# Performance work log

Hardware: AMD Instinct MI355X
Metric: run time of the kernel (lower is better)

Reference implementation:

```python
import jax, jax.numpy as jnp
import numpy as np

B, N, M, LDIM, RDIM, AGG = 4, 512, 512, 512, 512, 256


def setup_inputs() -> dict:
    key = jax.random.key(0)
    ks = jax.random.split(key, 7)
    data = jax.random.normal(ks[0], (B, N, LDIM), dtype=jnp.float32)
    crit = jax.random.normal(ks[1], (B, M, RDIM), dtype=jnp.float32)
    Wl = jax.random.normal(ks[2], (LDIM, AGG), dtype=jnp.float32) / np.sqrt(LDIM)
    bl = jax.random.normal(ks[3], (AGG,), dtype=jnp.float32) * 0.01
    Wr = jax.random.normal(ks[4], (RDIM, AGG), dtype=jnp.float32) / np.sqrt(RDIM)
    br = jax.random.normal(ks[5], (AGG,), dtype=jnp.float32) * 0.01
    agg = jax.random.uniform(ks[6], (AGG,), dtype=jnp.float32, minval=-0.01, maxval=0.01)
    return {"data": data, "crit": crit, "Wl": Wl, "bl": bl, "Wr": Wr, "br": br, "agg": agg}


def reference(data, crit, Wl, bl, Wr, br, agg):
    # linear projections
    datalin = jnp.einsum('bnl,la->bna', data, Wl) + bl   # [B,N,A]
    critlin = jnp.einsum('bmr,ra->bma', crit, Wr) + br   # [B,M,A]
    # broadcast add -> tanh -> reduce with agg vector: [B,N,M]
    linsum = jnp.tanh(datalin[:, :, None, :] + critlin[:, None, :, :])  # [B,N,M,A]
    dists = jnp.einsum('bnma,a->bnm', linsum, agg)
    return dists
```

## Files before the change

kernel.cpp:

```cpp
#include <hip/hip_runtime.h>


#define A_DIM 256
#define K_DIM 512
#define NROWS 2048

typedef unsigned short ushort;
typedef __attribute__((ext_vector_type(4))) unsigned short us4;

__device__ inline ushort f2bf(float x) {
    union { float f; unsigned u; } v; v.f = x;
    unsigned r = v.u + 0x7FFFu + ((v.u >> 16) & 1u);
    return (ushort)(r >> 16);
}
__device__ inline float bf2f(ushort h) {
    union { unsigned u; float f; } v; v.u = ((unsigned)h) << 16; return v.f;
}

__global__ __launch_bounds__(256) void proj_exp_kernel(
    const float* __restrict__ data, const float* __restrict__ crit,
    const float* __restrict__ Wl, const float* __restrict__ bl,
    const float* __restrict__ Wr, const float* __restrict__ br,
    ushort* __restrict__ ws16)
{
    __shared__ __align__(16) float Xs[16][68];
    __shared__ __align__(16) float Wsm[16][64];

    const int t   = threadIdx.x;
    const int bid = blockIdx.x;
    const int ct  = bid & 3;
    const int rt  = (bid >> 2) & 31;
    const int kh  = (bid >> 7) & 1;
    const int src = bid >> 8;

    const int r0 = rt * 64, c0 = ct * 64, kb = kh * 256;
    const float* X    = src ? crit : data;
    const float* W    = src ? Wr   : Wl;
    const float* bias = src ? br   : bl;
    ushort* ET = ws16 + (size_t)(src * 2 + kh) * ((size_t)A_DIM * NROWS);

    const int tx = t & 15;
    const int ty = t >> 4;
    const int sr = t >> 2;
    const int sk = (t & 3) * 4;
    const int wk = t >> 4;
    const int wc = (t & 15) * 4;

    float acc[4][4];
#pragma unroll
    for (int i = 0; i < 4; i++)
#pragma unroll
        for (int j = 0; j < 4; j++) acc[i][j] = 0.f;

    for (int k0 = 0; k0 < 256; k0 += 16) {
        float4 xv = *(const float4*)(X + (size_t)(r0 + sr) * K_DIM + kb + k0 + sk);
        float4 wv = *(const float4*)(W + (size_t)(kb + k0 + wk) * A_DIM + c0 + wc);
        __syncthreads();
        Xs[sk + 0][sr] = xv.x; Xs[sk + 1][sr] = xv.y;
        Xs[sk + 2][sr] = xv.z; Xs[sk + 3][sr] = xv.w;
        *(float4*)&Wsm[wk][wc] = wv;
        __syncthreads();
#pragma unroll
        for (int kk = 0; kk < 16; kk++) {
            float4 a4 = *(const float4*)&Xs[kk][ty * 4];
            float4 b4 = *(const float4*)&Wsm[kk][tx * 4];
            const float aa[4] = {a4.x, a4.y, a4.z, a4.w};
            const float bb[4] = {b4.x, b4.y, b4.z, b4.w};
#pragma unroll
            for (int i = 0; i < 4; i++)
#pragma unroll
                for (int j = 0; j < 4; j++)
                    acc[i][j] = fmaf(aa[i], bb[j], acc[i][j]);
        }
    }

    const float c2 = 2.8853900817779268f;
    float bvv[4] = {0.f, 0.f, 0.f, 0.f};
    if (kh == 0) {
        float4 bv = *(const float4*)(bias + c0 + tx * 4);
        bvv[0] = bv.x; bvv[1] = bv.y; bvv[2] = bv.z; bvv[3] = bv.w;
    }
#pragma unroll
    for (int j = 0; j < 4; j++) {
        us4 ev;
#pragma unroll
        for (int i = 0; i < 4; i++) {
            float v = (acc[i][j] + bvv[j]) * c2;
            v = fminf(fmaxf(v, -15.f), 15.f);
            ev[i] = f2bf(__builtin_amdgcn_exp2f(v));
        }
        *(us4*)(ET + (size_t)(c0 + tx * 4 + j) * NROWS + r0 + ty * 4) = ev;
    }
}

__global__ __launch_bounds__(256) void tanh_reduce_kernel(
    const ushort* __restrict__ ws16, const float* __restrict__ agg,
    float* __restrict__ partial)
{
    __shared__ __align__(16) float et [64][68];
    __shared__ __align__(16) float ect[64][68];
    __shared__ float aggs[128];

    const int t    = threadIdx.x;
    const int m0   = blockIdx.x * 64;
    const int n0   = blockIdx.y * 64;
    const int b    = blockIdx.z >> 1;
    const int half = blockIdx.z & 1;

    const size_t PLANE = (size_t)A_DIM * NROWS;
    const ushort* E1d = ws16;
    const ushort* E2d = ws16 + PLANE;
    const ushort* E1c = ws16 + 2 * PLANE;
    const ushort* E2c = ws16 + 3 * PLANE;
    const int row_n = b * 512 + n0;
    const int row_m = b * 512 + m0;

    const int tx = t & 15;
    const int ty = t >> 4;

    if (t < 128) aggs[t] = 2.0f * agg[half * 128 + t];

    float acc[4][4];
#pragma unroll
    for (int i = 0; i < 4; i++)
#pragma unroll
        for (int j = 0; j < 4; j++) acc[i][j] = 0.f;
    float sagg = 0.f;

    const int aL = t >> 2;
    const int qd = t & 3;

    for (int ch = 0; ch < 2; ch++) {
        const int a0 = half * 128 + ch * 64;
        __syncthreads();
#pragma unroll
        for (int r = 0; r < 4; r++) {
            const int seg = qd * 16 + r * 4;
            const size_t offn = (size_t)(a0 + aL) * NROWS + row_n + seg;
            const size_t offm = (size_t)(a0 + aL) * NROWS + row_m + seg;
            us4 d1 = *(const us4*)(E1d + offn);
            us4 d2 = *(const us4*)(E2d + offn);
            us4 c1 = *(const us4*)(E1c + offm);
            us4 c2 = *(const us4*)(E2c + offm);
            float4 ev, cv;
            ev.x = bf2f(d1[0]) * bf2f(d2[0]); ev.y = bf2f(d1[1]) * bf2f(d2[1]);
            ev.z = bf2f(d1[2]) * bf2f(d2[2]); ev.w = bf2f(d1[3]) * bf2f(d2[3]);
            cv.x = bf2f(c1[0]) * bf2f(c2[0]); cv.y = bf2f(c1[1]) * bf2f(c2[1]);
            cv.z = bf2f(c1[2]) * bf2f(c2[2]); cv.w = bf2f(c1[3]) * bf2f(c2[3]);
            *(float4*)&et [aL][seg] = ev;
            *(float4*)&ect[aL][seg] = cv;
        }
        __syncthreads();

        for (int p = 0; p < 32; p++) {
            const float2 ag = *(const float2*)&aggs[ch * 64 + p * 2];
            sagg += ag.x + ag.y;
            float4 e0 = *(const float4*)&et [p * 2 + 0][ty * 4];
            float4 e1 = *(const float4*)&et [p * 2 + 1][ty * 4];
            float4 f0 = *(const float4*)&ect[p * 2 + 0][tx * 4];
            float4 f1 = *(const float4*)&ect[p * 2 + 1][tx * 4];
            const float ea0[4] = {e0.x, e0.y, e0.z, e0.w};
            const float ea1[4] = {e1.x, e1.y, e1.z, e1.w};
            const float fa0[4] = {f0.x, f0.y, f0.z, f0.w};
            const float fa1[4] = {f1.x, f1.y, f1.z, f1.w};
#pragma unroll
            for (int i = 0; i < 4; i++)
#pragma unroll
                for (int j = 0; j < 4; j++) {
                    float q0 = fmaf(ea0[i], fa0[j], 1.f);
                    float q1 = fmaf(ea1[i], fa1[j], 1.f);
                    acc[i][j] = fmaf(fmaf(ag.x, q1, ag.y * q0),
                                     __builtin_amdgcn_rcpf(q0 * q1), acc[i][j]);
                }
        }
    }

    const float base = 0.5f * sagg;
    float* pl = partial + (size_t)half * (1 << 20);
#pragma unroll
    for (int i = 0; i < 4; i++) {
        float4 v;
        v.x = base - acc[i][0]; v.y = base - acc[i][1];
        v.z = base - acc[i][2]; v.w = base - acc[i][3];
        *(float4*)(pl + ((size_t)(b * 512 + n0 + ty * 4 + i) * 512) + m0 + tx * 4) = v;
    }
}

__global__ __launch_bounds__(256) void combine_kernel(
    const float* __restrict__ partial, float* __restrict__ out)
{
    const int idx = blockIdx.x * 256 + threadIdx.x;
    const float4* p0 = (const float4*)partial;
    const float4* p1 = (const float4*)(partial + (1 << 20));
    float4* o = (float4*)out;
#pragma unroll
    for (int r = 0; r < 2; r++) {
        const int i = idx + r * 131072;
        float4 a = p0[i], b = p1[i], v;
        v.x = a.x + b.x; v.y = a.y + b.y; v.z = a.z + b.z; v.w = a.w + b.w;
        o[i] = v;
    }
}

extern "C" void kernel_launch(void* const* d_in, const int* in_sizes, int n_in,
                              void* d_out, int out_size, void* d_ws, size_t ws_size,
                              hipStream_t stream) {
    const float* data = (const float*)d_in[0];
    const float* crit = (const float*)d_in[1];
    const float* Wl   = (const float*)d_in[2];
    const float* bl   = (const float*)d_in[3];
    const float* Wr   = (const float*)d_in[4];
    const float* br   = (const float*)d_in[5];
    const float* agg  = (const float*)d_in[6];
    float* out   = (float*)d_out;
    ushort* ws16 = (ushort*)d_ws;
    float* wspart = (float*)((char*)d_ws + 4u * 1024u * 1024u);

    proj_exp_kernel<<<dim3(512), 256, 0, stream>>>(data, crit, Wl, bl, Wr, br, ws16);

    tanh_reduce_kernel<<<dim3(8, 8, 8), 256, 0, stream>>>(ws16, agg, wspart);

    combine_kernel<<<dim3(512), 256, 0, stream>>>(wspart, out);
}
```

Measured before the change: 118.8 us.

## Compute projections with bf16 MFMA using pre-transposed bf16 weights

Replaces the fp32 SIMT projection GEMM, which was split over two K halves, with a bf16 MFMA kernel that covers the full K range in one pass. A new kernel first transposes the weights to bf16, and inputs are converted to bf16 on the fly. Because K is no longer split, the tanh-reduce kernel reads two exp planes instead of four and skips the elementwise products. This adds a kernel launch and lowers the precision of the input operands, and the changed rounding of the GEMM inputs may affect accuracy.

After: 113.0 us. 4.9% less time.

```diff
diff --git a/kernel.cpp b/kernel.cpp
--- a/kernel.cpp
+++ b/kernel.cpp
@@ -7,6 +7,9 @@
 
 typedef unsigned short ushort;
 typedef __attribute__((ext_vector_type(4))) unsigned short us4;
+typedef __attribute__((ext_vector_type(8))) unsigned short us8;
+typedef __attribute__((ext_vector_type(8))) short short8;
+typedef __attribute__((ext_vector_type(4))) float f32x4;
 
 __device__ inline ushort f2bf(float x) {
     union { float f; unsigned u; } v; v.f = x;
@@ -16,85 +19,129 @@
 __device__ inline float bf2f(ushort h) {
     union { unsigned u; float f; } v; v.u = ((unsigned)h) << 16; return v.f;
 }
-
-__global__ __launch_bounds__(256) void proj_exp_kernel(
+__device__ inline unsigned pack2bf(float lo, float hi) {
+    return (unsigned)f2bf(lo) | ((unsigned)f2bf(hi) << 16);
+}
+
+__global__ __launch_bounds__(256) void transpose_w_kernel(
+    const float* __restrict__ Wl, const float* __restrict__ Wr,
+    ushort* __restrict__ wt)
+{
+    __shared__ float tile[64][68];
+    const int t   = threadIdx.x;
+    const int bid = blockIdx.x;
+    const int at  = bid & 3;
+    const int kt  = (bid >> 2) & 7;
+    const int src = bid >> 5;
+    const int a0 = at * 64, k0 = kt * 64;
+    const float* W = src ? Wr : Wl;
+    ushort* out = wt + (size_t)src * (A_DIM * K_DIM);
+
+    const int c4 = (t & 15) * 4;
+    const int kr = t >> 4;
+#pragma unroll
+    for (int r = 0; r < 4; r++) {
+        const int k = kr + r * 16;
+        *(float4*)&tile[k][c4] = *(const float4*)(W + (size_t)(k0 + k) * A_DIM + a0 + c4);
+    }
+    __syncthreads();
+    const int aL  = t & 63;
+    const int ks0 = (t >> 6) * 16;
+#pragma unroll
+    for (int g = 0; g < 4; g++) {
+        us4 o;
+#pragma unroll
+        for (int i = 0; i < 4; i++) o[i] = f2bf(tile[ks0 + g * 4 + i][aL]);
+        *(us4*)(out + (size_t)(a0 + aL) * K_DIM + k0 + ks0 + g * 4) = o;
+    }
+}
+
+__global__ __launch_bounds__(256) void proj_mfma_kernel(
     const float* __restrict__ data, const float* __restrict__ crit,
-    const float* __restrict__ Wl, const float* __restrict__ bl,
-    const float* __restrict__ Wr, const float* __restrict__ br,
-    ushort* __restrict__ ws16)
-{
-    __shared__ __align__(16) float Xs[16][68];
-    __shared__ __align__(16) float Wsm[16][64];
+    const float* __restrict__ bl, const float* __restrict__ br,
+    const ushort* __restrict__ wt, ushort* __restrict__ eplanes)
+{
+    __shared__ ushort Ws[64][264];
 
     const int t   = threadIdx.x;
     const int bid = blockIdx.x;
     const int ct  = bid & 3;
-    const int rt  = (bid >> 2) & 31;
-    const int kh  = (bid >> 7) & 1;
-    const int src = bid >> 8;
-
-    const int r0 = rt * 64, c0 = ct * 64, kb = kh * 256;
+    const int rt  = bid >> 2;
+    const int src = rt >> 6;
+    const int lr0 = (rt & 63) * 32;
+    const int c0  = ct * 64;
+
     const float* X    = src ? crit : data;
-    const float* W    = src ? Wr   : Wl;
-    const float* bias = src ? br   : bl;
-    ushort* ET = ws16 + (size_t)(src * 2 + kh) * ((size_t)A_DIM * NROWS);
-
-    const int tx = t & 15;
-    const int ty = t >> 4;
-    const int sr = t >> 2;
-    const int sk = (t & 3) * 4;
-    const int wk = t >> 4;
-    const int wc = (t & 15) * 4;
-
-    float acc[4][4];
-#pragma unroll
-    for (int i = 0; i < 4; i++)
-#pragma unroll
-        for (int j = 0; j < 4; j++) acc[i][j] = 0.f;
-
-    for (int k0 = 0; k0 < 256; k0 += 16) {
-        float4 xv = *(const float4*)(X + (size_t)(r0 + sr) * K_DIM + kb + k0 + sk);
-        float4 wv = *(const float4*)(W + (size_t)(kb + k0 + wk) * A_DIM + c0 + wc);
-        __syncthreads();
-        Xs[sk + 0][sr] = xv.x; Xs[sk + 1][sr] = xv.y;
-        Xs[sk + 2][sr] = xv.z; Xs[sk + 3][sr] = xv.w;
-        *(float4*)&Wsm[wk][wc] = wv;
-        __syncthreads();
-#pragma unroll
-        for (int kk = 0; kk < 16; kk++) {
-            float4 a4 = *(const float4*)&Xs[kk][ty * 4];
-            float4 b4 = *(const float4*)&Wsm[kk][tx * 4];
-            const float aa[4] = {a4.x, a4.y, a4.z, a4.w};
-            const float bb[4] = {b4.x, b4.y, b4.z, b4.w};
-#pragma unroll
-            for (int i = 0; i < 4; i++)
-#pragma unroll
-                for (int j = 0; j < 4; j++)
-                    acc[i][j] = fmaf(aa[i], bb[j], acc[i][j]);
+    const float* bias = src ? br : bl;
+    const ushort* Wt  = wt + (size_t)src * (A_DIM * K_DIM);
+    ushort* E = eplanes + (size_t)src * ((size_t)A_DIM * NROWS);
+
+    const int lane = t & 63;
+    const int wid  = t >> 6;
+    const int wm   = wid >> 1, wn = wid & 1;
+    const int quad = lane >> 4, l16 = lane & 15;
+
+    const float* xrow = X + (size_t)(lr0 + wm * 16 + l16) * K_DIM + quad * 8;
+    const int aloc0 = wn * 32 + l16;
+
+    f32x4 acc0 = {0.f, 0.f, 0.f, 0.f}, acc1 = {0.f, 0.f, 0.f, 0.f};
+
+    float4 pa = *(const float4*)(xrow);
+    float4 pb = *(const float4*)(xrow + 4);
+
+    for (int kc = 0; kc < 2; kc++) {
+        __syncthreads();
+        {
+            const int a  = t & 63;
+            const int ks = (t >> 6) * 64;
+            const ushort* s = Wt + (size_t)(c0 + a) * K_DIM + kc * 256 + ks;
+#pragma unroll
+            for (int i = 0; i < 8; i++)
+                *(us8*)&Ws[a][ks + i * 8] = *(const us8*)(s + i * 8);
+        }
+        __syncthreads();
+
+#pragma unroll
+        for (int ls = 0; ls < 8; ls++) {
+            const int s = kc * 8 + ls;
+            float4 ca = pa, cb = pb;
+            if (s < 15) {
+                pa = *(const float4*)(xrow + (s + 1) * 32);
+                pb = *(const float4*)(xrow + (s + 1) * 32 + 4);
+            }
+            union { short8 s8; unsigned u[4]; } af;
+            af.u[0] = pack2bf(ca.x, ca.y);
+            af.u[1] = pack2bf(ca.z, ca.w);
+            af.u[2] = pack2bf(cb.x, cb.y);
+            af.u[3] = pack2bf(cb.z, cb.w);
+            short8 b0 = *(const short8*)&Ws[aloc0     ][ls * 32 + quad * 8];
+            short8 b1 = *(const short8*)&Ws[aloc0 + 16][ls * 32 + quad * 8];
+            acc0 = __builtin_amdgcn_mfma_f32_16x16x32_bf16(af.s8, b0, acc0, 0, 0, 0);
+            acc1 = __builtin_amdgcn_mfma_f32_16x16x32_bf16(af.s8, b1, acc1, 0, 0, 0);
         }
     }
 
     const float c2 = 2.8853900817779268f;
-    float bvv[4] = {0.f, 0.f, 0.f, 0.f};
-    if (kh == 0) {
-        float4 bv = *(const float4*)(bias + c0 + tx * 4);
-        bvv[0] = bv.x; bvv[1] = bv.y; bvv[2] = bv.z; bvv[3] = bv.w;
-    }
-#pragma unroll
-    for (int j = 0; j < 4; j++) {
-        us4 ev;
-#pragma unroll
-        for (int i = 0; i < 4; i++) {
-            float v = (acc[i][j] + bvv[j]) * c2;
-            v = fminf(fmaxf(v, -15.f), 15.f);
-            ev[i] = f2bf(__builtin_amdgcn_exp2f(v));
-        }
-        *(us4*)(ET + (size_t)(c0 + tx * 4 + j) * NROWS + r0 + ty * 4) = ev;
-    }
+    const int a_col0 = c0 + wn * 32 + l16;
+    const int a_col1 = a_col0 + 16;
+    const int row0   = lr0 + wm * 16 + quad * 4;
+    const float bv0 = bias[a_col0], bv1 = bias[a_col1];
+    us4 e0, e1;
+#pragma unroll
+    for (int i = 0; i < 4; i++) {
+        float v0 = (acc0[i] + bv0) * c2;
+        float v1 = (acc1[i] + bv1) * c2;
+        v0 = fminf(fmaxf(v0, -15.f), 15.f);
+        v1 = fminf(fmaxf(v1, -15.f), 15.f);
+        e0[i] = f2bf(__builtin_amdgcn_exp2f(v0));
+        e1[i] = f2bf(__builtin_amdgcn_exp2f(v1));
+    }
+    *(us4*)(E + (size_t)a_col0 * NROWS + row0) = e0;
+    *(us4*)(E + (size_t)a_col1 * NROWS + row0) = e1;
 }
 
 __global__ __launch_bounds__(256) void tanh_reduce_kernel(
-    const ushort* __restrict__ ws16, const float* __restrict__ agg,
+    const ushort* __restrict__ eplanes, const float* __restrict__ agg,
     float* __restrict__ partial)
 {
     __shared__ __align__(16) float et [64][68];
@@ -108,10 +155,8 @@
     const int half = blockIdx.z & 1;
 
     const size_t PLANE = (size_t)A_DIM * NROWS;
-    const ushort* E1d = ws16;
-    const ushort* E2d = ws16 + PLANE;
-    const ushort* E1c = ws16 + 2 * PLANE;
-    const ushort* E2c = ws16 + 3 * PLANE;
+    const ushort* Ed = eplanes;
+    const ushort* Ec = eplanes + PLANE;
     const int row_n = b * 512 + n0;
     const int row_m = b * 512 + m0;
 
@@ -136,17 +181,11 @@
 #pragma unroll
         for (int r = 0; r < 4; r++) {
             const int seg = qd * 16 + r * 4;
-            const size_t offn = (size_t)(a0 + aL) * NROWS + row_n + seg;
-            const size_t offm = (size_t)(a0 + aL) * NROWS + row_m + seg;
-            us4 d1 = *(const us4*)(E1d + offn);
-            us4 d2 = *(const us4*)(E2d + offn);
-            us4 c1 = *(const us4*)(E1c + offm);
-            us4 c2 = *(const us4*)(E2c + offm);
+            us4 d = *(const us4*)(Ed + (size_t)(a0 + aL) * NROWS + row_n + seg);
+            us4 c = *(const us4*)(Ec + (size_t)(a0 + aL) * NROWS + row_m + seg);
             float4 ev, cv;
-            ev.x = bf2f(d1[0]) * bf2f(d2[0]); ev.y = bf2f(d1[1]) * bf2f(d2[1]);
-            ev.z = bf2f(d1[2]) * bf2f(d2[2]); ev.w = bf2f(d1[3]) * bf2f(d2[3]);
-            cv.x = bf2f(c1[0]) * bf2f(c2[0]); cv.y = bf2f(c1[1]) * bf2f(c2[1]);
-            cv.z = bf2f(c1[2]) * bf2f(c2[2]); cv.w = bf2f(c1[3]) * bf2f(c2[3]);
+            ev.x = bf2f(d[0]); ev.y = bf2f(d[1]); ev.z = bf2f(d[2]); ev.w = bf2f(d[3]);
+            cv.x = bf2f(c[0]); cv.y = bf2f(c[1]); cv.z = bf2f(c[2]); cv.w = bf2f(c[3]);
             *(float4*)&et [aL][seg] = ev;
             *(float4*)&ect[aL][seg] = cv;
         }
@@ -212,13 +251,18 @@
     const float* Wr   = (const float*)d_in[4];
     const float* br   = (const float*)d_in[5];
     const float* agg  = (const float*)d_in[6];
-    float* out   = (float*)d_out;
+    float* out = (float*)d_out;
+
     ushort* ws16 = (ushort*)d_ws;
-    float* wspart = (float*)((char*)d_ws + 4u * 1024u * 1024u);
-
-    proj_exp_kernel<<<dim3(512), 256, 0, stream>>>(data, crit, Wl, bl, Wr, br, ws16);
-
-    tanh_reduce_kernel<<<dim3(8, 8, 8), 256, 0, stream>>>(ws16, agg, wspart);
+    ushort* eplanes = ws16;
+    ushort* wt      = ws16 + 2 * (size_t)A_DIM * NROWS;
+    float* wspart   = (float*)((char*)d_ws + 8u * 1024u * 1024u);
+
+    transpose_w_kernel<<<dim3(64), 256, 0, stream>>>(Wl, Wr, wt);
+
+    proj_mfma_kernel<<<dim3(512), 256, 0, stream>>>(data, crit, bl, br, wt, eplanes);
+
+    tanh_reduce_kernel<<<dim3(8, 8, 8), 256, 0, stream>>>(eplanes, agg, wspart);
 
     combine_kernel<<<dim3(512), 256, 0, stream>>>(wspart, out);
 }
```
